# Kernel optimization log

Measured on AMD Instinct MI355X. Metric: run time of the kernel, lower is better.

The kernel has to match this reference:

```python
import jax, jax.numpy as jnp
import numpy as np

R = 10      # brain regions (graph nodes)
C = 6       # channels per region
HID = 128   # hidden_dim
HEADS = 4   # GAT heads (concat=False -> mean over heads)
L = 3       # num_gnn_layers
EPS = 1e-5  # LayerNorm eps
NEG_SLOPE = 0.2  # GATConv leaky_relu slope

_REGIONS = ['prefrontal','premotor','primary_motor','primary_sensory','somatic_sensory',
            'broca','wernicke','auditory','auditory_assoc','visual']


def _build_edges():
    idx = {n: i for i, n in enumerate(_REGIONS)}
    edges = [('wernicke','broca'), ('broca','primary_motor'), ('visual','wernicke'),
             ('visual','prefrontal'), ('prefrontal','broca'), ('prefrontal','wernicke'),
             ('prefrontal','premotor'), ('premotor','primary_motor'),
             ('primary_motor','primary_sensory'), ('auditory','wernicke'),
             ('auditory','broca'), ('auditory_assoc','auditory'),
             ('somatic_sensory','primary_sensory')]
    src, dst = [], []
    for s, d in edges:
        src += [idx[s], idx[d]]
        dst += [idx[d], idx[s]]
    for i in range(R):  # self loops (GATConv add_self_loops nets out to one per node)
        src.append(i); dst.append(i)
    return np.array(src, np.int32), np.array(dst, np.int32)


def setup_inputs() -> dict:
    key = jax.random.key(0)
    ks = jax.random.split(key, 10)
    x = jax.random.normal(ks[0], (16, 800, R * C), dtype=jnp.float32)
    # per-region encoder: Linear(C->HID) + LayerNorm(HID), stacked over regions
    Wenc  = jax.random.normal(ks[1], (R, C, HID), dtype=jnp.float32) * 0.1
    benc  = jnp.zeros((R, HID), dtype=jnp.float32)
    gamma = jnp.ones((R, HID), dtype=jnp.float32)
    beta  = jnp.zeros((R, HID), dtype=jnp.float32)
    # GATConv params per layer: lin (no bias), att_src/att_dst, output bias
    Wg   = jax.random.normal(ks[2], (L, HID, HEADS * HID), dtype=jnp.float32) * 0.05
    asrc = jax.random.normal(ks[3], (L, HEADS, HID), dtype=jnp.float32) * 0.1
    adst = jax.random.normal(ks[4], (L, HEADS, HID), dtype=jnp.float32) * 0.1
    bg   = jnp.zeros((L, HID), dtype=jnp.float32)
    src_np, dst_np = _build_edges()
    return {'x': x, 'Wenc': Wenc, 'benc': benc, 'gamma': gamma, 'beta': beta,
            'Wg': Wg, 'asrc': asrc, 'adst': adst, 'bg': bg,
            'src': jnp.asarray(src_np), 'dst': jnp.asarray(dst_np)}


def _gat_layer(nf, W, a_src, a_dst, bias, src, dst):
    # nf: (B,T,R,HID). PyG GATConv, heads=HEADS, concat=False.
    B, T, _, _ = nf.shape
    xp = jnp.einsum('btnf,fk->btnk', nf, W).reshape(B, T, R, HEADS, HID)
    al_s = jnp.einsum('btnhf,hf->btnh', xp, a_src)   # (B,T,R,H)
    al_d = jnp.einsum('btnhf,hf->btnh', xp, a_dst)
    e = al_s[:, :, src] + al_d[:, :, dst]            # (B,T,E,H)
    e = jnp.where(e > 0, e, NEG_SLOPE * e)           # leaky_relu
    # segment softmax over edges grouped by destination node
    e_t = jnp.moveaxis(e, 2, 0)                      # (E,B,T,H)
    m = jax.ops.segment_max(e_t, dst, num_segments=R)
    ex = jnp.exp(e_t - m[dst])
    s = jax.ops.segment_sum(ex, dst, num_segments=R)
    alpha = ex / s[dst]                              # (E,B,T,H)
    msg = xp[:, :, src] * jnp.moveaxis(alpha, 0, 2)[..., None]  # (B,T,E,H,F)
    agg = jax.ops.segment_sum(jnp.moveaxis(msg, 2, 0), dst, num_segments=R)  # (R,B,T,H,F)
    out = jnp.moveaxis(agg, 0, 2).mean(axis=3) + bias            # (B,T,R,HID)
    return out


def reference(x, Wenc, benc, gamma, beta, Wg, asrc, adst, bg, src, dst):
    B, T, _ = x.shape
    xr = x.reshape(B, T, R, C)
    h = jnp.einsum('btrc,rch->btrh', xr, Wenc) + benc
    mu = h.mean(-1, keepdims=True)
    var = h.var(-1, keepdims=True)
    h = (h - mu) / jnp.sqrt(var + EPS) * gamma + beta
    region_feats = jax.nn.gelu(h, approximate=False)  # (B,T,R,HID)
    nf = region_feats
    for l in range(L):
        residual = nf
        nf = _gat_layer(nf, Wg[l], asrc[l], adst[l], bg[l], src, dst)
        nf = jax.nn.gelu(nf, approximate=False) + residual  # dropout = identity (eval)
    graph_features = nf.reshape(B, T, R * HID)
    return graph_features, region_feats
```

## Files before the change

### kernel.cpp

```cpp
#include <hip/hip_runtime.h>
#include <hip/hip_bf16.h>
#include <math.h>

#define R 10
#define C 6
#define HID 128
#define HEADS 4
#define NL 3
#define KO 512
#define TOK 1280
#define NCAT 544
#define NT 33
#define NUSE 520
#define XPH 528
#define HS 132
#define NFS 136
#define LN_EPS 1e-5f
#define NEG_SLOPE 0.2f
#define MAXE 40
#define MAXDEG 16

typedef __attribute__((ext_vector_type(8))) short short8;
typedef __attribute__((ext_vector_type(4))) float floatx4;
typedef _Float16 half4v __attribute__((ext_vector_type(4)));

__device__ __forceinline__ float gelu_exact(float v) {
    return 0.5f * v * (1.0f + erff(v * 0.70710678118654752440f));
}
__device__ __forceinline__ short f2bf(float v) {
    __hip_bfloat16 b = __float2bfloat16(v);
    return __builtin_bit_cast(short, b);
}

__global__ void prep_wcat(const float* __restrict__ Wg,
                          const float* __restrict__ asrc,
                          const float* __restrict__ adst,
                          short* __restrict__ Wcat)
{
    int idx = blockIdx.x * 256 + threadIdx.x;
    const int TOTAL = NL * NCAT * HID;
    if (idx >= TOTAL) return;
    int k = idx & (HID - 1);
    int n = (idx >> 7) % NCAT;
    int l = idx / (NCAT * HID);
    float v = 0.f;
    if (n < KO) {
        v = Wg[((size_t)l * HID + k) * KO + n];
    } else if (n < KO + 8) {
        int h = (n - KO) & 3;
        const float* a = ((n - KO) < 4 ? asrc : adst) + (l * HEADS + h) * HID;
        const float* w = Wg + ((size_t)l * HID + k) * KO + h * HID;
        float s = 0.f;
        for (int f = 0; f < HID; ++f) s = fmaf(w[f], a[f], s);
        v = s;
    }
    Wcat[idx] = f2bf(v);
}

__global__ __launch_bounds__(256, 5) void fused_gnn_mfma(
    const float* __restrict__ x,
    const float* __restrict__ Wenc,
    const float* __restrict__ benc,
    const float* __restrict__ gamma_,
    const float* __restrict__ beta_,
    const short* __restrict__ Wcat,
    const float* __restrict__ bg,
    const int* __restrict__ srce, const int* __restrict__ dste,
    float* __restrict__ gf_out, float* __restrict__ rf_out, int E)
{
    __shared__ __align__(16) char s_big[2 * R * XPH * 2];
    __shared__ __align__(16) short s_nfb[2 * R * NFS];
    __shared__ float s_un[320];
    __shared__ float s_logit[2 * R * 8];
    __shared__ int s_src[MAXE], s_dst[MAXE];
    __shared__ int s_eid[R * MAXDEG], s_deg[R];

    float* s_h = reinterpret_cast<float*>(s_big);
    _Float16* s_xph = reinterpret_cast<_Float16*>(s_big);

    const int t = threadIdx.x;
    const int lane = t & 63;
    const int wave = t >> 6;
    const int tok0 = blockIdx.x * 2;

    if (t < E) { s_src[t] = srce[t]; s_dst[t] = dste[t]; }
    if (t < 120) s_un[t] = x[(size_t)tok0 * 60 + t];
    __syncthreads();
    if (t < R) {
        int d = 0;
        for (int e = 0; e < E; ++e)
            if (s_dst[e] == t && d < MAXDEG) s_eid[t * MAXDEG + (d++)] = e;
        s_deg[t] = d;
    }

    for (int q = t; q < 640; q += 256) {
        int tk = q >= 320; int qq = q - tk * 320;
        int r = qq >> 5; int f4 = (qq & 31) << 2;
        const float* xr = &s_un[tk * 60 + r * 6];
        float4 acc = *(const float4*)&benc[r * HID + f4];
        #pragma unroll
        for (int c = 0; c < 6; ++c) {
            float xv = xr[c];
            float4 wv = *(const float4*)&Wenc[(r * 6 + c) * HID + f4];
            acc.x = fmaf(xv, wv.x, acc.x);
            acc.y = fmaf(xv, wv.y, acc.y);
            acc.z = fmaf(xv, wv.z, acc.z);
            acc.w = fmaf(xv, wv.w, acc.w);
        }
        *(float4*)&s_h[(tk * R + r) * HS + f4] = acc;
    }
    __syncthreads();

    for (int rr = wave; rr < 20; rr += 4) {
        const float* row = &s_h[rr * HS];
        float v0 = row[lane], v1 = row[lane + 64];
        float sum = v0 + v1, sq = v0 * v0 + v1 * v1;
        #pragma unroll
        for (int off = 32; off > 0; off >>= 1) {
            sum += __shfl_down(sum, off);
            sq  += __shfl_down(sq,  off);
        }
        if (lane == 0) {
            float mu = sum * (1.0f / HID);
            float var = sq * (1.0f / HID) - mu * mu;
            s_un[128 + rr] = mu;
            s_un[148 + rr] = rsqrtf(var + LN_EPS);
        }
    }
    __syncthreads();

    float4 nf_reg[3];
    {
        int nq = 0;
        for (int q = t; q < 640; q += 256, ++nq) {
            int tk = q >= 320; int qq = q - tk * 320;
            int r = qq >> 5; int f4 = (qq & 31) << 2;
            float4 v = *(const float4*)&s_h[(tk * R + r) * HS + f4];
            float mu = s_un[128 + tk * 10 + r];
            float rs = s_un[148 + tk * 10 + r];
            float4 g = *(const float4*)&gamma_[r * HID + f4];
            float4 b = *(const float4*)&beta_[r * HID + f4];
            float4 o;
            o.x = gelu_exact((v.x - mu) * rs * g.x + b.x);
            o.y = gelu_exact((v.y - mu) * rs * g.y + b.y);
            o.z = gelu_exact((v.z - mu) * rs * g.z + b.z);
            o.w = gelu_exact((v.w - mu) * rs * g.w + b.w);
            nf_reg[nq] = o;
            short4 pk; pk.x = f2bf(o.x); pk.y = f2bf(o.y); pk.z = f2bf(o.z); pk.w = f2bf(o.w);
            *(short4*)&s_nfb[(tk * R + r) * NFS + f4] = pk;
            *(float4*)&rf_out[(size_t)(tok0 + tk) * TOK + qq * 4] = o;
        }
    }
    __syncthreads();

    const int col = lane & 15;
    const int quad = lane >> 4;
    const int aoff = quad * 8;
    const int crow = (col < R) ? col : 0;

    for (int l = 0; l < NL; ++l) {
        const short* __restrict__ Wl = Wcat + (size_t)l * NCAT * HID;

        short8 aF[2][4];
        #pragma unroll
        for (int tk = 0; tk < 2; ++tk)
            #pragma unroll
            for (int ks = 0; ks < 4; ++ks)
                aF[tk][ks] = *(const short8*)&s_nfb[(tk * R + crow) * NFS + ks * 32 + aoff];

        for (int nt = wave; nt < NT; nt += 4) {
            const short* Bp = Wl + (nt * 16 + col) * HID + aoff;
            short8 b0 = *(const short8*)(Bp);
            short8 b1 = *(const short8*)(Bp + 32);
            short8 b2 = *(const short8*)(Bp + 64);
            short8 b3 = *(const short8*)(Bp + 96);
            int n = nt * 16 + col;
            #pragma unroll
            for (int tk = 0; tk < 2; ++tk) {
                floatx4 c = {0.f, 0.f, 0.f, 0.f};
                c = __builtin_amdgcn_mfma_f32_16x16x32_bf16(aF[tk][0], b0, c, 0, 0, 0);
                c = __builtin_amdgcn_mfma_f32_16x16x32_bf16(aF[tk][1], b1, c, 0, 0, 0);
                c = __builtin_amdgcn_mfma_f32_16x16x32_bf16(aF[tk][2], b2, c, 0, 0, 0);
                c = __builtin_amdgcn_mfma_f32_16x16x32_bf16(aF[tk][3], b3, c, 0, 0, 0);
                if (n < KO) {
                    #pragma unroll
                    for (int j = 0; j < 4; ++j) {
                        int m = quad * 4 + j;
                        if (m < R) s_xph[(tk * R + m) * XPH + n] = (_Float16)c[j];
                    }
                } else if (n < NUSE) {
                    #pragma unroll
                    for (int j = 0; j < 4; ++j) {
                        int m = quad * 4 + j;
                        if (m < R) s_logit[(tk * R + m) * 8 + (n - KO)] = c[j];
                    }
                }
            }
        }
        __syncthreads();

        if (t < 80) {
            int tk = t / 40; int rem = t - tk * 40;
            int r = rem >> 2; int h = rem & 3;
            const float* lg = &s_logit[tk * R * 8];
            float ald = lg[r * 8 + 4 + h];
            int d = s_deg[r];
            float m = -1e30f;
            for (int k = 0; k < d; ++k) {
                int e = s_eid[r * MAXDEG + k];
                float val = lg[s_src[e] * 8 + h] + ald;
                val = (val > 0.f) ? val : NEG_SLOPE * val;
                m = fmaxf(m, val);
            }
            float ssum = 0.f;
            for (int k = 0; k < d; ++k) {
                int e = s_eid[r * MAXDEG + k];
                float val = lg[s_src[e] * 8 + h] + ald;
                val = (val > 0.f) ? val : NEG_SLOPE * val;
                ssum += expf(val - m);
            }
            float inv = 1.0f / ssum;
            for (int k = 0; k < d; ++k) {
                int e = s_eid[r * MAXDEG + k];
                float val = lg[s_src[e] * 8 + h] + ald;
                val = (val > 0.f) ? val : NEG_SLOPE * val;
                s_un[(tk * 40 + e) * 4 + h] = expf(val - m) * inv;
            }
        }
        __syncthreads();

        {
            int nq = 0;
            for (int q = t; q < 640; q += 256, ++nq) {
                int tk = q >= 320; int qq = q - tk * 320;
                int r = qq >> 5; int f4 = (qq & 31) << 2;
                float4 acc = {0.f, 0.f, 0.f, 0.f};
                int d = s_deg[r];
                const _Float16* xb = &s_xph[tk * R * XPH];
                for (int k = 0; k < d; ++k) {
                    int e = s_eid[r * MAXDEG + k];
                    const _Float16* row = xb + s_src[e] * XPH;
                    #pragma unroll
                    for (int h = 0; h < 4; ++h) {
                        float a = s_un[(tk * 40 + e) * 4 + h];
                        half4v xv = *(const half4v*)&row[h * HID + f4];
                        acc.x = fmaf(a, (float)xv.x, acc.x);
                        acc.y = fmaf(a, (float)xv.y, acc.y);
                        acc.z = fmaf(a, (float)xv.z, acc.z);
                        acc.w = fmaf(a, (float)xv.w, acc.w);
                    }
                }
                float4 bb = *(const float4*)&bg[l * HID + f4];
                float4 o;
                o.x = gelu_exact(acc.x * 0.25f + bb.x) + nf_reg[nq].x;
                o.y = gelu_exact(acc.y * 0.25f + bb.y) + nf_reg[nq].y;
                o.z = gelu_exact(acc.z * 0.25f + bb.z) + nf_reg[nq].z;
                o.w = gelu_exact(acc.w * 0.25f + bb.w) + nf_reg[nq].w;
                nf_reg[nq] = o;
                if (l < NL - 1) {
                    short4 pk; pk.x = f2bf(o.x); pk.y = f2bf(o.y); pk.z = f2bf(o.z); pk.w = f2bf(o.w);
                    *(short4*)&s_nfb[(tk * R + r) * NFS + f4] = pk;
                }
            }
        }
        __syncthreads();
    }

    {
        int nq = 0;
        for (int q = t; q < 640; q += 256, ++nq) {
            int tk = q >= 320; int qq = q - tk * 320;
            *(float4*)&gf_out[(size_t)(tok0 + tk) * TOK + qq * 4] = nf_reg[nq];
        }
    }
}

extern "C" void kernel_launch(void* const* d_in, const int* in_sizes, int n_in,
                              void* d_out, int out_size, void* d_ws, size_t ws_size,
                              hipStream_t stream) {
    const float* x      = (const float*)d_in[0];
    const float* Wenc   = (const float*)d_in[1];
    const float* benc   = (const float*)d_in[2];
    const float* gamma_ = (const float*)d_in[3];
    const float* beta_  = (const float*)d_in[4];
    const float* Wg     = (const float*)d_in[5];
    const float* asrc   = (const float*)d_in[6];
    const float* adst   = (const float*)d_in[7];
    const float* bg     = (const float*)d_in[8];
    const int*   srce   = (const int*)d_in[9];
    const int*   dste   = (const int*)d_in[10];

    const int E  = in_sizes[9];
    const int BT = in_sizes[0] / (R * C);

    float* gf = (float*)d_out;
    float* rf = gf + (size_t)BT * TOK;
    short* Wcat = (short*)d_ws;

    const int prep_total = NL * NCAT * HID;
    prep_wcat<<<(prep_total + 255) / 256, 256, 0, stream>>>(Wg, asrc, adst, Wcat);
    fused_gnn_mfma<<<BT / 2, 256, 0, stream>>>(x, Wenc, benc, gamma_, beta_,
                                               Wcat, bg, srce, dste, gf, rf, E);
}
```

Baseline: 496.4 us.

## Aggregate GAT messages with MFMA using a dense alpha matrix held in registers

```diff
diff --git a/kernel.cpp b/kernel.cpp
--- a/kernel.cpp
+++ b/kernel.cpp
@@ -10,19 +10,17 @@
 #define KO 512
 #define TOK 1280
 #define NCAT 544
-#define NT 33
-#define NUSE 520
-#define XPH 528
 #define HS 132
 #define NFS 136
+#define AS 20
 #define LN_EPS 1e-5f
 #define NEG_SLOPE 0.2f
 #define MAXE 40
-#define MAXDEG 16
+#define MAXDEG 8
 
 typedef __attribute__((ext_vector_type(8))) short short8;
 typedef __attribute__((ext_vector_type(4))) float floatx4;
-typedef _Float16 half4v __attribute__((ext_vector_type(4)));
+typedef _Float16 half4 __attribute__((ext_vector_type(4)));
 
 __device__ __forceinline__ float gelu_exact(float v) {
     return 0.5f * v * (1.0f + erff(v * 0.70710678118654752440f));
@@ -57,7 +55,7 @@
     Wcat[idx] = f2bf(v);
 }
 
-__global__ __launch_bounds__(256, 5) void fused_gnn_mfma(
+__global__ __launch_bounds__(256, 6) void fused_gnn_mfma(
     const float* __restrict__ x,
     const float* __restrict__ Wenc,
     const float* __restrict__ benc,
@@ -68,15 +66,13 @@
     const int* __restrict__ srce, const int* __restrict__ dste,
     float* __restrict__ gf_out, float* __restrict__ rf_out, int E)
 {
-    __shared__ __align__(16) char s_big[2 * R * XPH * 2];
+    __shared__ __align__(16) float s_h[2 * R * HS];
     __shared__ __align__(16) short s_nfb[2 * R * NFS];
-    __shared__ float s_un[320];
+    __shared__ __align__(16) _Float16 s_alpha[2 * HEADS * 16 * AS];
+    __shared__ float s_un[168];
     __shared__ float s_logit[2 * R * 8];
     __shared__ int s_src[MAXE], s_dst[MAXE];
     __shared__ int s_eid[R * MAXDEG], s_deg[R];
-
-    float* s_h = reinterpret_cast<float*>(s_big);
-    _Float16* s_xph = reinterpret_cast<_Float16*>(s_big);
 
     const int t = threadIdx.x;
     const int lane = t & 63;
@@ -168,34 +164,55 @@
             for (int ks = 0; ks < 4; ++ks)
                 aF[tk][ks] = *(const short8*)&s_nfb[(tk * R + crow) * NFS + ks * 32 + aoff];
 
-        for (int nt = wave; nt < NT; nt += 4) {
-            const short* Bp = Wl + (nt * 16 + col) * HID + aoff;
+        half4 xF[2][HEADS][2];
+        #pragma unroll
+        for (int h = 0; h < HEADS; ++h) {
+            #pragma unroll
+            for (int j = 0; j < 2; ++j) {
+                int tile = h * 8 + 2 * wave + j;
+                const short* Bp = Wl + (tile * 16 + col) * HID + aoff;
+                short8 b0 = *(const short8*)(Bp);
+                short8 b1 = *(const short8*)(Bp + 32);
+                short8 b2 = *(const short8*)(Bp + 64);
+                short8 b3 = *(const short8*)(Bp + 96);
+                #pragma unroll
+                for (int tk = 0; tk < 2; ++tk) {
+                    floatx4 c = {0.f, 0.f, 0.f, 0.f};
+                    c = __builtin_amdgcn_mfma_f32_16x16x32_bf16(aF[tk][0], b0, c, 0, 0, 0);
+                    c = __builtin_amdgcn_mfma_f32_16x16x32_bf16(aF[tk][1], b1, c, 0, 0, 0);
+                    c = __builtin_amdgcn_mfma_f32_16x16x32_bf16(aF[tk][2], b2, c, 0, 0, 0);
+                    c = __builtin_amdgcn_mfma_f32_16x16x32_bf16(aF[tk][3], b3, c, 0, 0, 0);
+                    half4 xf;
+                    xf[0] = (_Float16)c[0]; xf[1] = (_Float16)c[1];
+                    xf[2] = (_Float16)c[2]; xf[3] = (_Float16)c[3];
+                    xF[tk][h][j] = xf;
+                }
+            }
+        }
+        if (wave < 2) {
+            const short* Bp = Wl + (KO + col) * HID + aoff;
             short8 b0 = *(const short8*)(Bp);
             short8 b1 = *(const short8*)(Bp + 32);
             short8 b2 = *(const short8*)(Bp + 64);
             short8 b3 = *(const short8*)(Bp + 96);
-            int n = nt * 16 + col;
-            #pragma unroll
-            for (int tk = 0; tk < 2; ++tk) {
-                floatx4 c = {0.f, 0.f, 0.f, 0.f};
-                c = __builtin_amdgcn_mfma_f32_16x16x32_bf16(aF[tk][0], b0, c, 0, 0, 0);
-                c = __builtin_amdgcn_mfma_f32_16x16x32_bf16(aF[tk][1], b1, c, 0, 0, 0);
-                c = __builtin_amdgcn_mfma_f32_16x16x32_bf16(aF[tk][2], b2, c, 0, 0, 0);
-                c = __builtin_amdgcn_mfma_f32_16x16x32_bf16(aF[tk][3], b3, c, 0, 0, 0);
-                if (n < KO) {
-                    #pragma unroll
-                    for (int j = 0; j < 4; ++j) {
-                        int m = quad * 4 + j;
-                        if (m < R) s_xph[(tk * R + m) * XPH + n] = (_Float16)c[j];
-                    }
-                } else if (n < NUSE) {
-                    #pragma unroll
-                    for (int j = 0; j < 4; ++j) {
-                        int m = quad * 4 + j;
-                        if (m < R) s_logit[(tk * R + m) * 8 + (n - KO)] = c[j];
-                    }
+            int tk = wave;
+            floatx4 c = {0.f, 0.f, 0.f, 0.f};
+            c = __builtin_amdgcn_mfma_f32_16x16x32_bf16(aF[tk][0], b0, c, 0, 0, 0);
+            c = __builtin_amdgcn_mfma_f32_16x16x32_bf16(aF[tk][1], b1, c, 0, 0, 0);
+            c = __builtin_amdgcn_mfma_f32_16x16x32_bf16(aF[tk][2], b2, c, 0, 0, 0);
+            c = __builtin_amdgcn_mfma_f32_16x16x32_bf16(aF[tk][3], b3, c, 0, 0, 0);
+            if (col < 8) {
+                #pragma unroll
+                for (int j = 0; j < 4; ++j) {
+                    int m = quad * 4 + j;
+                    if (m < R) s_logit[(tk * R + m) * 8 + col] = c[j];
                 }
             }
+        }
+        {
+            int* pa = (int*)s_alpha;
+            #pragma unroll
+            for (int i = t; i < 2 * HEADS * 16 * AS / 2; i += 256) pa[i] = 0;
         }
         __syncthreads();
 
@@ -222,9 +239,33 @@
             float inv = 1.0f / ssum;
             for (int k = 0; k < d; ++k) {
                 int e = s_eid[r * MAXDEG + k];
-                float val = lg[s_src[e] * 8 + h] + ald;
+                int s = s_src[e];
+                float val = lg[s * 8 + h] + ald;
                 val = (val > 0.f) ? val : NEG_SLOPE * val;
-                s_un[(tk * 40 + e) * 4 + h] = expf(val - m) * inv;
+                s_alpha[((tk * HEADS + h) * 16 + r) * AS + s] = (_Float16)(expf(val - m) * inv);
+            }
+        }
+        __syncthreads();
+
+        half4 alF[2][HEADS];
+        #pragma unroll
+        for (int tk = 0; tk < 2; ++tk)
+            #pragma unroll
+            for (int h = 0; h < HEADS; ++h)
+                alF[tk][h] = *(const half4*)&s_alpha[((tk * HEADS + h) * 16 + col) * AS + quad * 4];
+        #pragma unroll
+        for (int tk = 0; tk < 2; ++tk) {
+            #pragma unroll
+            for (int jt = 0; jt < 2; ++jt) {
+                floatx4 o = {0.f, 0.f, 0.f, 0.f};
+                #pragma unroll
+                for (int h = 0; h < HEADS; ++h)
+                    o = __builtin_amdgcn_mfma_f32_16x16x16f16(alF[tk][h], xF[tk][h][jt], o, 0, 0, 0);
+                #pragma unroll
+                for (int j = 0; j < 4; ++j) {
+                    int m = quad * 4 + j;
+                    if (m < R) s_h[(tk * R + m) * HS + wave * 32 + jt * 16 + col] = o[j];
+                }
             }
         }
         __syncthreads();
@@ -234,22 +275,7 @@
             for (int q = t; q < 640; q += 256, ++nq) {
                 int tk = q >= 320; int qq = q - tk * 320;
                 int r = qq >> 5; int f4 = (qq & 31) << 2;
-                float4 acc = {0.f, 0.f, 0.f, 0.f};
-                int d = s_deg[r];
-                const _Float16* xb = &s_xph[tk * R * XPH];
-                for (int k = 0; k < d; ++k) {
-                    int e = s_eid[r * MAXDEG + k];
-                    const _Float16* row = xb + s_src[e] * XPH;
-                    #pragma unroll
-                    for (int h = 0; h < 4; ++h) {
-                        float a = s_un[(tk * 40 + e) * 4 + h];
-                        half4v xv = *(const half4v*)&row[h * HID + f4];
-                        acc.x = fmaf(a, (float)xv.x, acc.x);
-                        acc.y = fmaf(a, (float)xv.y, acc.y);
-                        acc.z = fmaf(a, (float)xv.z, acc.z);
-                        acc.w = fmaf(a, (float)xv.w, acc.w);
-                    }
-                }
+                float4 acc = *(const float4*)&s_h[(tk * R + r) * HS + f4];
                 float4 bb = *(const float4*)&bg[l * HID + f4];
                 float4 o;
                 o.x = gelu_exact(acc.x * 0.25f + bb.x) + nf_reg[nq].x;
```

After: 790.7 us. 1.59x slower.

## Process one token per 128-thread block instead of two per 256-thread block

Applied to the files above, without the earlier changes.

```diff
diff --git a/kernel.cpp b/kernel.cpp
--- a/kernel.cpp
+++ b/kernel.cpp
@@ -12,13 +12,13 @@
 #define NCAT 544
 #define NT 33
 #define NUSE 520
-#define XPH 528
-#define HS 132
+#define XPH 524
+#define HSF 132
 #define NFS 136
 #define LN_EPS 1e-5f
 #define NEG_SLOPE 0.2f
 #define MAXE 40
-#define MAXDEG 16
+#define MAXDEG 8
 
 typedef __attribute__((ext_vector_type(8))) short short8;
 typedef __attribute__((ext_vector_type(4))) float floatx4;
@@ -57,7 +57,7 @@
     Wcat[idx] = f2bf(v);
 }
 
-__global__ __launch_bounds__(256, 5) void fused_gnn_mfma(
+__global__ __launch_bounds__(128, 5) void fused_gnn_mfma(
     const float* __restrict__ x,
     const float* __restrict__ Wenc,
     const float* __restrict__ benc,
@@ -68,10 +68,10 @@
     const int* __restrict__ srce, const int* __restrict__ dste,
     float* __restrict__ gf_out, float* __restrict__ rf_out, int E)
 {
-    __shared__ __align__(16) char s_big[2 * R * XPH * 2];
-    __shared__ __align__(16) short s_nfb[2 * R * NFS];
-    __shared__ float s_un[320];
-    __shared__ float s_logit[2 * R * 8];
+    __shared__ __align__(16) char s_big[R * XPH * 2];
+    __shared__ __align__(16) short s_nfb[R * NFS];
+    __shared__ float s_un[168];
+    __shared__ float s_logit[R * 8];
     __shared__ int s_src[MAXE], s_dst[MAXE];
     __shared__ int s_eid[R * MAXDEG], s_deg[R];
 
@@ -81,10 +81,10 @@
     const int t = threadIdx.x;
     const int lane = t & 63;
     const int wave = t >> 6;
-    const int tok0 = blockIdx.x * 2;
+    const int tok = blockIdx.x;
 
     if (t < E) { s_src[t] = srce[t]; s_dst[t] = dste[t]; }
-    if (t < 120) s_un[t] = x[(size_t)tok0 * 60 + t];
+    if (t < 60) s_un[t] = x[(size_t)tok * 60 + t];
     __syncthreads();
     if (t < R) {
         int d = 0;
@@ -93,10 +93,9 @@
         s_deg[t] = d;
     }
 
-    for (int q = t; q < 640; q += 256) {
-        int tk = q >= 320; int qq = q - tk * 320;
-        int r = qq >> 5; int f4 = (qq & 31) << 2;
-        const float* xr = &s_un[tk * 60 + r * 6];
+    for (int q = t; q < 320; q += 128) {
+        int r = q >> 5; int f4 = (q & 31) << 2;
+        const float* xr = &s_un[r * 6];
         float4 acc = *(const float4*)&benc[r * HID + f4];
         #pragma unroll
         for (int c = 0; c < 6; ++c) {
@@ -107,12 +106,12 @@
             acc.z = fmaf(xv, wv.z, acc.z);
             acc.w = fmaf(xv, wv.w, acc.w);
         }
-        *(float4*)&s_h[(tk * R + r) * HS + f4] = acc;
-    }
-    __syncthreads();
-
-    for (int rr = wave; rr < 20; rr += 4) {
-        const float* row = &s_h[rr * HS];
+        *(float4*)&s_h[r * HSF + f4] = acc;
+    }
+    __syncthreads();
+
+    for (int rr = wave; rr < R; rr += 2) {
+        const float* row = &s_h[rr * HSF];
         float v0 = row[lane], v1 = row[lane + 64];
         float sum = v0 + v1, sq = v0 * v0 + v1 * v1;
         #pragma unroll
@@ -123,8 +122,8 @@
         if (lane == 0) {
             float mu = sum * (1.0f / HID);
             float var = sq * (1.0f / HID) - mu * mu;
-            s_un[128 + rr] = mu;
-            s_un[148 + rr] = rsqrtf(var + LN_EPS);
+            s_un[64 + rr] = mu;
+            s_un[80 + rr] = rsqrtf(var + LN_EPS);
         }
     }
     __syncthreads();
@@ -132,12 +131,11 @@
     float4 nf_reg[3];
     {
         int nq = 0;
-        for (int q = t; q < 640; q += 256, ++nq) {
-            int tk = q >= 320; int qq = q - tk * 320;
-            int r = qq >> 5; int f4 = (qq & 31) << 2;
-            float4 v = *(const float4*)&s_h[(tk * R + r) * HS + f4];
-            float mu = s_un[128 + tk * 10 + r];
-            float rs = s_un[148 + tk * 10 + r];
+        for (int q = t; q < 320; q += 128, ++nq) {
+            int r = q >> 5; int f4 = (q & 31) << 2;
+            float4 v = *(const float4*)&s_h[r * HSF + f4];
+            float mu = s_un[64 + r];
+            float rs = s_un[80 + r];
             float4 g = *(const float4*)&gamma_[r * HID + f4];
             float4 b = *(const float4*)&beta_[r * HID + f4];
             float4 o;
@@ -147,8 +145,8 @@
             o.w = gelu_exact((v.w - mu) * rs * g.w + b.w);
             nf_reg[nq] = o;
             short4 pk; pk.x = f2bf(o.x); pk.y = f2bf(o.y); pk.z = f2bf(o.z); pk.w = f2bf(o.w);
-            *(short4*)&s_nfb[(tk * R + r) * NFS + f4] = pk;
-            *(float4*)&rf_out[(size_t)(tok0 + tk) * TOK + qq * 4] = o;
+            *(short4*)&s_nfb[r * NFS + f4] = pk;
+            *(float4*)&rf_out[(size_t)tok * TOK + q * 4] = o;
         }
     }
     __syncthreads();
@@ -161,88 +159,79 @@
     for (int l = 0; l < NL; ++l) {
         const short* __restrict__ Wl = Wcat + (size_t)l * NCAT * HID;
 
-        short8 aF[2][4];
+        short8 aF[4];
         #pragma unroll
-        for (int tk = 0; tk < 2; ++tk)
-            #pragma unroll
-            for (int ks = 0; ks < 4; ++ks)
-                aF[tk][ks] = *(const short8*)&s_nfb[(tk * R + crow) * NFS + ks * 32 + aoff];
-
-        for (int nt = wave; nt < NT; nt += 4) {
+        for (int ks = 0; ks < 4; ++ks)
+            aF[ks] = *(const short8*)&s_nfb[crow * NFS + ks * 32 + aoff];
+
+        for (int nt = wave; nt < NT; nt += 2) {
             const short* Bp = Wl + (nt * 16 + col) * HID + aoff;
             short8 b0 = *(const short8*)(Bp);
             short8 b1 = *(const short8*)(Bp + 32);
             short8 b2 = *(const short8*)(Bp + 64);
             short8 b3 = *(const short8*)(Bp + 96);
             int n = nt * 16 + col;
-            #pragma unroll
-            for (int tk = 0; tk < 2; ++tk) {
-                floatx4 c = {0.f, 0.f, 0.f, 0.f};
-                c = __builtin_amdgcn_mfma_f32_16x16x32_bf16(aF[tk][0], b0, c, 0, 0, 0);
-                c = __builtin_amdgcn_mfma_f32_16x16x32_bf16(aF[tk][1], b1, c, 0, 0, 0);
-                c = __builtin_amdgcn_mfma_f32_16x16x32_bf16(aF[tk][2], b2, c, 0, 0, 0);
-                c = __builtin_amdgcn_mfma_f32_16x16x32_bf16(aF[tk][3], b3, c, 0, 0, 0);
-                if (n < KO) {
-                    #pragma unroll
-                    for (int j = 0; j < 4; ++j) {
-                        int m = quad * 4 + j;
-                        if (m < R) s_xph[(tk * R + m) * XPH + n] = (_Float16)c[j];
-                    }
-                } else if (n < NUSE) {
-                    #pragma unroll
-                    for (int j = 0; j < 4; ++j) {
-                        int m = quad * 4 + j;
-                        if (m < R) s_logit[(tk * R + m) * 8 + (n - KO)] = c[j];
-                    }
+            floatx4 c = {0.f, 0.f, 0.f, 0.f};
+            c = __builtin_amdgcn_mfma_f32_16x16x32_bf16(aF[0], b0, c, 0, 0, 0);
+            c = __builtin_amdgcn_mfma_f32_16x16x32_bf16(aF[1], b1, c, 0, 0, 0);
+            c = __builtin_amdgcn_mfma_f32_16x16x32_bf16(aF[2], b2, c, 0, 0, 0);
+            c = __builtin_amdgcn_mfma_f32_16x16x32_bf16(aF[3], b3, c, 0, 0, 0);
+            if (n < KO) {
+                #pragma unroll
+                for (int j = 0; j < 4; ++j) {
+                    int m = quad * 4 + j;
+                    if (m < R) s_xph[m * XPH + n] = (_Float16)c[j];
+                }
+            } else if (n < NUSE) {
+                #pragma unroll
+                for (int j = 0; j < 4; ++j) {
+                    int m = quad * 4 + j;
+                    if (m < R) s_logit[m * 8 + (n - KO)] = c[j];
                 }
             }
         }
         __syncthreads();
 
-        if (t < 80) {
-            int tk = t / 40; int rem = t - tk * 40;
-            int r = rem >> 2; int h = rem & 3;
-            const float* lg = &s_logit[tk * R * 8];
-            float ald = lg[r * 8 + 4 + h];
+        if (t < 40) {
+            int r = t >> 2; int h = t & 3;
+            float ald = s_logit[r * 8 + 4 + h];
             int d = s_deg[r];
             float m = -1e30f;
             for (int k = 0; k < d; ++k) {
                 int e = s_eid[r * MAXDEG + k];
-                float val = lg[s_src[e] * 8 + h] + ald;
+                float val = s_logit[s_src[e] * 8 + h] + ald;
                 val = (val > 0.f) ? val : NEG_SLOPE * val;
                 m = fmaxf(m, val);
             }
             float ssum = 0.f;
             for (int k = 0; k < d; ++k) {
                 int e = s_eid[r * MAXDEG + k];
-                float val = lg[s_src[e] * 8 + h] + ald;
+                float val = s_logit[s_src[e] * 8 + h] + ald;
                 val = (val > 0.f) ? val : NEG_SLOPE * val;
                 ssum += expf(val - m);
             }
             float inv = 1.0f / ssum;
             for (int k = 0; k < d; ++k) {
                 int e = s_eid[r * MAXDEG + k];
-                float val = lg[s_src[e] * 8 + h] + ald;
+                float val = s_logit[s_src[e] * 8 + h] + ald;
                 val = (val > 0.f) ? val : NEG_SLOPE * val;
-                s_un[(tk * 40 + e) * 4 + h] = expf(val - m) * inv;
+                s_un[e * 4 + h] = expf(val - m) * inv;
             }
         }
         __syncthreads();
 
         {
             int nq = 0;
-            for (int q = t; q < 640; q += 256, ++nq) {
-                int tk = q >= 320; int qq = q - tk * 320;
-                int r = qq >> 5; int f4 = (qq & 31) << 2;
+            for (int q = t; q < 320; q += 128, ++nq) {
+                int r = q >> 5; int f4 = (q & 31) << 2;
                 float4 acc = {0.f, 0.f, 0.f, 0.f};
                 int d = s_deg[r];
-                const _Float16* xb = &s_xph[tk * R * XPH];
                 for (int k = 0; k < d; ++k) {
                     int e = s_eid[r * MAXDEG + k];
-                    const _Float16* row = xb + s_src[e] * XPH;
+                    const _Float16* row = s_xph + s_src[e] * XPH;
                     #pragma unroll
                     for (int h = 0; h < 4; ++h) {
-                        float a = s_un[(tk * 40 + e) * 4 + h];
+                        float a = s_un[e * 4 + h];
                         half4v xv = *(const half4v*)&row[h * HID + f4];
                         acc.x = fmaf(a, (float)xv.x, acc.x);
                         acc.y = fmaf(a, (float)xv.y, acc.y);
@@ -259,19 +248,16 @@
                 nf_reg[nq] = o;
                 if (l < NL - 1) {
                     short4 pk; pk.x = f2bf(o.x); pk.y = f2bf(o.y); pk.z = f2bf(o.z); pk.w = f2bf(o.w);
-                    *(short4*)&s_nfb[(tk * R + r) * NFS + f4] = pk;
+                    *(short4*)&s_nfb[r * NFS + f4] = pk;
                 }
             }
         }
         __syncthreads();
     }
 
-    {
-        int nq = 0;
-        for (int q = t; q < 640; q += 256, ++nq) {
-            int tk = q >= 320; int qq = q - tk * 320;
-            *(float4*)&gf_out[(size_t)(tok0 + tk) * TOK + qq * 4] = nf_reg[nq];
-        }
+    for (int q = t; q < 320; q += 128) {
+        int nq = (q - t) / 128;
+        *(float4*)&gf_out[(size_t)tok * TOK + q * 4] = nf_reg[nq];
     }
 }
 
@@ -299,6 +285,6 @@
 
     const int prep_total = NL * NCAT * HID;
     prep_wcat<<<(prep_total + 255) / 256, 256, 0, stream>>>(Wg, asrc, adst, Wcat);
-    fused_gnn_mfma<<<BT / 2, 256, 0, stream>>>(x, Wenc, benc, gamma_, beta_,
-                                               Wcat, bg, srce, dste, gf, rf, E);
-}
+    fused_gnn_mfma<<<BT, 128, 0, stream>>>(x, Wenc, benc, gamma_, beta_,
+                                           Wcat, bg, srce, dste, gf, rf, E);
+}
```

Result: slower. 750.6 us (+51.2%).
